# Performance work log

Measured on AMD Instinct MI355X. Metric: run time of the kernel, lower is better.

The kernel has to match this reference:

```python
import jax, jax.numpy as jnp
import numpy as np

N_DST = 50000


def setup_inputs() -> dict:
    key = jax.random.key(0)
    k1, k2, k3, k4, k5, k6 = jax.random.split(key, 6)
    n_src, n_dst, n_edges, d_in, d_out = 50000, 50000, 1600000, 128, 128
    return {
        "h_neigh": jax.random.normal(k1, (n_src, d_in), dtype=jnp.float32),
        "h_self": jax.random.normal(k2, (n_dst, d_in), dtype=jnp.float32),
        "src_idx": jax.random.randint(k3, (n_edges,), 0, n_src, dtype=jnp.int32),
        "dst_idx": jax.random.randint(k4, (n_edges,), 0, n_dst, dtype=jnp.int32),
        "W_self": jax.random.normal(k5, (d_out, d_in), dtype=jnp.float32) * 0.05,
        "W_neigh": jax.random.normal(k6, (d_out, d_in), dtype=jnp.float32) * 0.05,
    }


def reference(h_neigh, h_self, src_idx, dst_idx, W_self, W_neigh):
    # mean aggregation over edges: for each dst node, mean of src features
    msgs = h_neigh[src_idx]                                   # [E, d_in]
    summed = jax.ops.segment_sum(msgs, dst_idx, num_segments=N_DST)  # [N_dst, d_in]
    deg = jax.ops.segment_sum(jnp.ones_like(dst_idx, dtype=h_neigh.dtype),
                              dst_idx, num_segments=N_DST)    # [N_dst]
    agg = summed / jnp.maximum(deg, 1.0)[:, None]             # mean; 0 for isolated nodes

    z = h_self @ W_self.T + agg @ W_neigh.T                   # [N_dst, d_out]
    z = jax.nn.relu(z)
    # L2 normalize rows, guarding zero norms
    z_norm = jnp.linalg.norm(z, axis=1, keepdims=True)
    z_norm = jnp.where(z_norm == 0, 1.0, z_norm)
    return z / z_norm
```

## Files before the change

kernel.cpp:

```cpp
#include <hip/hip_runtime.h>
#include <hip/hip_bf16.h>

#define DFEAT 128
#define BSH 7
#define CAP 4608

typedef short short8 __attribute__((ext_vector_type(8)));
typedef float f32x4 __attribute__((ext_vector_type(4)));

__global__ void prep_kernel(const float2* __restrict__ in, __hip_bfloat162* __restrict__ out,
                            int n2, int nconv,
                            const float* __restrict__ Wself, const float* __restrict__ Wneigh,
                            unsigned short* __restrict__ wcat, int* __restrict__ gcursor) {
    int b = blockIdx.x;
    int tid = threadIdx.x;
    if (b < nconv) {
        int i = b * 256 + tid;
        if (i < n2) {
            float2 v = in[i];
            __hip_bfloat162 o;
            o.x = __float2bfloat16(v.x);
            o.y = __float2bfloat16(v.y);
            out[i] = o;
        }
    } else {
        int bb = b - nconv;
        int idx = bb * 256 + tid;
        int j = idx >> 8, k = idx & 255;
        float v = (k < DFEAT) ? Wself[j * DFEAT + k] : Wneigh[j * DFEAT + k - DFEAT];
        __hip_bfloat16 h = __float2bfloat16(v);
        wcat[idx] = *(unsigned short*)&h;
        if (bb < 2) {
            int s = bb * 256 + tid;
            gcursor[s] = s * CAP;
        }
    }
}

__global__ void partition_kernel(const int* __restrict__ src, const int* __restrict__ dst,
                                 int E, int* __restrict__ gcursor,
                                 unsigned* __restrict__ pairs) {
    __shared__ int hist[512];
    __shared__ int base[512];
    int tid = threadIdx.x;
    for (int b0 = blockIdx.x * 2048; b0 < E; b0 += gridDim.x * 2048) {
        hist[tid] = 0;
        hist[tid + 256] = 0;
        __syncthreads();
        unsigned mypk[8];
        int mybin[8], myrank[8];
#pragma unroll
        for (int e = 0; e < 8; ++e) {
            int i = b0 + e * 256 + tid;
            mybin[e] = -1;
            if (i < E) {
                unsigned d = (unsigned)dst[i];
                unsigned s = (unsigned)src[i];
                int bin = d >> BSH;
                mybin[e] = bin;
                myrank[e] = atomicAdd(&hist[bin], 1);
                mypk[e] = (d << 16) | s;
            }
        }
        __syncthreads();
        if (hist[tid]) base[tid] = atomicAdd(&gcursor[tid], hist[tid]);
        if (hist[tid + 256]) base[tid + 256] = atomicAdd(&gcursor[tid + 256], hist[tid + 256]);
        __syncthreads();
#pragma unroll
        for (int e = 0; e < 8; ++e)
            if (mybin[e] >= 0) pairs[base[mybin[e]] + myrank[e]] = mypk[e];
        __syncthreads();
    }
}

__global__ void fine_fill_kernel(const unsigned* __restrict__ pairs,
                                 const int* __restrict__ gcursor,
                                 int* __restrict__ row_start, int* __restrict__ deg,
                                 unsigned short* __restrict__ csr16, int n_dst) {
    __shared__ int hist[256];
    __shared__ int cur[256];
    __shared__ int wtot[4];
    int b = blockIdx.x;
    int tid = threadIdx.x;
    int lo = b * CAP, hi = gcursor[b];
    hist[tid] = 0;
    __syncthreads();
    for (int j = lo + tid; j < hi; j += 256)
        atomicAdd(&hist[(pairs[j] >> 16) & 127], 1);
    __syncthreads();
    int v = hist[tid];
    int lane = tid & 63, w = tid >> 6;
    int x = v;
    for (int off = 1; off < 64; off <<= 1) {
        int t = __shfl_up(x, off);
        if (lane >= off) x += t;
    }
    if (lane == 63) wtot[w] = x;
    __syncthreads();
    if (tid == 0) {
        int r = 0;
        for (int i = 0; i < 4; ++i) { int t = wtot[i]; wtot[i] = r; r += t; }
    }
    __syncthreads();
    int excl = x + wtot[w] - v;
    cur[tid] = excl;
    int d = (b << BSH) + tid;
    if (tid < (1 << BSH) && d < n_dst) {
        row_start[d] = lo + excl;
        deg[d] = v;
    }
    __syncthreads();
    for (int j = lo + tid; j < hi; j += 256) {
        unsigned p = pairs[j];
        int slot = atomicAdd(&cur[(p >> 16) & 127], 1);
        csr16[lo + slot] = (unsigned short)(p & 0xFFFFu);
    }
}

template <int PASS>
__global__ void aggregate_kernel(const unsigned short* __restrict__ hnb,
                                 const unsigned short* __restrict__ csr16,
                                 const int* __restrict__ row_start,
                                 const int* __restrict__ deg,
                                 unsigned short* __restrict__ agb, int n_dst) {
    int gtid = blockIdx.x * blockDim.x + threadIdx.x;
    int d = gtid >> 6;
    if (d >= n_dst) return;
    int lane = threadIdx.x & 63;
    int beg = row_start[d];
    int dg = deg[d];
    int slot = lane >> 4;
    int fg = lane & 15;
    const unsigned short* tab = hnb + PASS * 64 + fg * 4;
    float a0 = 0.f, a1 = 0.f, a2 = 0.f, a3 = 0.f;
    for (int base = 0; base < dg; base += 64) {
        int cnt = dg - base;
        if (cnt > 64) cnt = 64;
        int s = (base + lane < dg) ? (int)csr16[beg + base + lane] : 0;
        for (int j = 0; j < cnt; j += 8) {
            int e0 = j + slot;
            int e1 = e0 + 4;
            int i0 = __shfl(s, e0);
            int i1 = __shfl(s, e1 & 63);
            ushort4 v0 = *(const ushort4*)(tab + i0 * DFEAT);
            ushort4 v1 = *(const ushort4*)(tab + i1 * DFEAT);
            if (e0 < cnt) {
                a0 += __bfloat162float(*(__hip_bfloat16*)&v0.x);
                a1 += __bfloat162float(*(__hip_bfloat16*)&v0.y);
                a2 += __bfloat162float(*(__hip_bfloat16*)&v0.z);
                a3 += __bfloat162float(*(__hip_bfloat16*)&v0.w);
            }
            if (e1 < cnt) {
                a0 += __bfloat162float(*(__hip_bfloat16*)&v1.x);
                a1 += __bfloat162float(*(__hip_bfloat16*)&v1.y);
                a2 += __bfloat162float(*(__hip_bfloat16*)&v1.z);
                a3 += __bfloat162float(*(__hip_bfloat16*)&v1.w);
            }
        }
    }
    a0 += __shfl_xor(a0, 16); a0 += __shfl_xor(a0, 32);
    a1 += __shfl_xor(a1, 16); a1 += __shfl_xor(a1, 32);
    a2 += __shfl_xor(a2, 16); a2 += __shfl_xor(a2, 32);
    a3 += __shfl_xor(a3, 16); a3 += __shfl_xor(a3, 32);
    if (lane < 16) {
        float inv = 1.0f / (float)(dg > 1 ? dg : 1);
        __hip_bfloat16 b0 = __float2bfloat16(a0 * inv);
        __hip_bfloat16 b1 = __float2bfloat16(a1 * inv);
        __hip_bfloat16 b2 = __float2bfloat16(a2 * inv);
        __hip_bfloat16 b3 = __float2bfloat16(a3 * inv);
        ushort4 o;
        o.x = *(unsigned short*)&b0;
        o.y = *(unsigned short*)&b1;
        o.z = *(unsigned short*)&b2;
        o.w = *(unsigned short*)&b3;
        *(ushort4*)(agb + d * DFEAT + PASS * 64 + lane * 4) = o;
    }
}

__launch_bounds__(512, 4)
__global__ void gemm_mfma_kernel(const float* __restrict__ h_self,
                                 const unsigned short* __restrict__ agb,
                                 const unsigned short* __restrict__ Wcat,
                                 float* __restrict__ out, int M) {
    __shared__ char Ws[64 * 1024];
    int tid = threadIdx.x;
    int row0 = blockIdx.x * 128;
    {
        int j = tid >> 2, q = tid & 3;
#pragma unroll
        for (int u = 0; u < 8; ++u) {
            int ks = q * 64 + u * 8;
            uint4 vv = *(const uint4*)(Wcat + j * 256 + ks);
            *(uint4*)(Ws + ((j * 512 + ks * 2) ^ ((j & 7) << 4))) = vv;
        }
    }
    __syncthreads();

    int lane = tid & 63, w = tid >> 6;
    int arow = row0 + w * 16 + (lane & 15);
    int kgrp = (lane >> 4) * 8;
    bool rv = arow < M;
    int ar = rv ? arow : 0;

    f32x4 acc[8] = {};
#pragma unroll
    for (int kstep = 0; kstep < 8; ++kstep) {
        int kk = kstep * 32 + kgrp;
        short8 a;
        if (kk < DFEAT) {
            float4 f0 = *(const float4*)(h_self + (size_t)ar * DFEAT + kk);
            float4 f1 = *(const float4*)(h_self + (size_t)ar * DFEAT + kk + 4);
            __hip_bfloat16 b0 = __float2bfloat16(f0.x), b1 = __float2bfloat16(f0.y);
            __hip_bfloat16 b2 = __float2bfloat16(f0.z), b3 = __float2bfloat16(f0.w);
            __hip_bfloat16 b4 = __float2bfloat16(f1.x), b5 = __float2bfloat16(f1.y);
            __hip_bfloat16 b6 = __float2bfloat16(f1.z), b7 = __float2bfloat16(f1.w);
            a[0] = *(short*)&b0; a[1] = *(short*)&b1; a[2] = *(short*)&b2; a[3] = *(short*)&b3;
            a[4] = *(short*)&b4; a[5] = *(short*)&b5; a[6] = *(short*)&b6; a[7] = *(short*)&b7;
        } else {
            a = *(const short8*)(agb + (size_t)ar * DFEAT + (kk - DFEAT));
        }
#pragma unroll
        for (int n = 0; n < 8; ++n) {
            int nr = n * 16 + (lane & 15);
            short8 bfrag = *(const short8*)(Ws + ((nr * 512 + kk * 2) ^ ((nr & 7) << 4)));
            acc[n] = __builtin_amdgcn_mfma_f32_16x16x32_bf16(a, bfrag, acc[n], 0, 0, 0);
        }
    }

    float ss[4] = {0.f, 0.f, 0.f, 0.f};
#pragma unroll
    for (int n = 0; n < 8; ++n)
#pragma unroll
        for (int i = 0; i < 4; ++i) {
            float z = fmaxf(acc[n][i], 0.f);
            acc[n][i] = z;
            ss[i] += z * z;
        }
#pragma unroll
    for (int i = 0; i < 4; ++i)
        for (int m = 1; m < 16; m <<= 1) ss[i] += __shfl_xor(ss[i], m);
#pragma unroll
    for (int i = 0; i < 4; ++i) {
        int grow = row0 + w * 16 + (lane >> 4) * 4 + i;
        if (grow < M) {
            float nv = sqrtf(ss[i]);
            float inv = (nv == 0.f) ? 1.f : 1.f / nv;
#pragma unroll
            for (int n = 0; n < 8; ++n)
                out[(size_t)grow * DFEAT + n * 16 + (lane & 15)] = acc[n][i] * inv;
        }
    }
}

extern "C" void kernel_launch(void* const* d_in, const int* in_sizes, int n_in,
                              void* d_out, int out_size, void* d_ws, size_t ws_size,
                              hipStream_t stream) {
    const float* h_neigh = (const float*)d_in[0];
    const float* h_self  = (const float*)d_in[1];
    const int*   src_idx = (const int*)d_in[2];
    const int*   dst_idx = (const int*)d_in[3];
    const float* W_self  = (const float*)d_in[4];
    const float* W_neigh = (const float*)d_in[5];
    float* out = (float*)d_out;

    const int D = DFEAT;
    int n_src = in_sizes[0] / D;
    int n_dst = in_sizes[1] / D;
    int E = in_sizes[2];
    int NB = (n_dst + (1 << BSH) - 1) >> BSH;

    char* wsp = (char*)d_ws;
    size_t off = 0;
    auto alloc = [&](size_t bytes) -> void* {
        void* p = wsp + off;
        off += (bytes + 255) & ~(size_t)255;
        return p;
    };
    int* gcursor          = (int*)alloc(512 * 4);
    int* row_start        = (int*)alloc((size_t)n_dst * 4);
    int* deg              = (int*)alloc((size_t)n_dst * 4);
    unsigned* pairs       = (unsigned*)alloc((size_t)NB * CAP * 4);
    unsigned short* csr16 = (unsigned short*)alloc((size_t)NB * CAP * 2 + 256);
    unsigned short* hnb   = (unsigned short*)alloc((size_t)n_src * D * 2);
    unsigned short* agb   = (unsigned short*)alloc((size_t)n_dst * D * 2);
    unsigned short* wcat  = (unsigned short*)alloc((size_t)DFEAT * 256 * 2);
    (void)ws_size;

    int n2 = n_src * (D / 2);
    int nconv = (n2 + 255) / 256;
    prep_kernel<<<nconv + 128, 256, 0, stream>>>(
        (const float2*)h_neigh, (__hip_bfloat162*)hnb, n2, nconv,
        W_self, W_neigh, wcat, gcursor);

    partition_kernel<<<256, 256, 0, stream>>>(src_idx, dst_idx, E, gcursor, pairs);

    fine_fill_kernel<<<NB, 256, 0, stream>>>(pairs, gcursor, row_start, deg, csr16, n_dst);

    int agg_blocks = (n_dst * 64 + 255) / 256;
    aggregate_kernel<0><<<agg_blocks, 256, 0, stream>>>(hnb, csr16, row_start, deg, agb, n_dst);
    aggregate_kernel<1><<<agg_blocks, 256, 0, stream>>>(hnb, csr16, row_start, deg, agb, n_dst);

    gemm_mfma_kernel<<<(n_dst + 127) / 128, 512, 0, stream>>>(
        h_self, agb, wcat, out, n_dst);
}
```

Before: 130.4 us.

## Widen aggregate gathers to 16-byte loads with zero-row padding; vectorize partition index loads

The aggregate kernel now has each lane gather 8 bf16 features (16 bytes) instead of 4, with 8 edge slots per wavefront and four independent gathers per iteration. Padded edge slots point at an appended all-zero row of the bf16 neighbor table, so per-edge bounds branches disappear. The partition kernel reads src/dst as int4 vectors with contiguous per-thread edge ranges instead of strided scalar loads. This trades more wasted gather work on padded slots and higher register use for fewer, wider memory transactions and more memory-level parallelism.

```diff
diff --git a/kernel.cpp b/kernel.cpp
--- a/kernel.cpp
+++ b/kernel.cpp
@@ -6,10 +6,11 @@
 #define CAP 4608
 
 typedef short short8 __attribute__((ext_vector_type(8)));
+typedef unsigned short ushort8 __attribute__((ext_vector_type(8)));
 typedef float f32x4 __attribute__((ext_vector_type(4)));
 
 __global__ void prep_kernel(const float2* __restrict__ in, __hip_bfloat162* __restrict__ out,
-                            int n2, int nconv,
+                            int n2, int nconv, int n_src,
                             const float* __restrict__ Wself, const float* __restrict__ Wneigh,
                             unsigned short* __restrict__ wcat, int* __restrict__ gcursor) {
     int b = blockIdx.x;
@@ -34,6 +35,9 @@
             int s = bb * 256 + tid;
             gcursor[s] = s * CAP;
         }
+        if (bb == 2 && tid < DFEAT) {
+            ((unsigned short*)out)[(size_t)n_src * DFEAT + tid] = 0;
+        }
     }
 }
 
@@ -47,19 +51,36 @@
         hist[tid] = 0;
         hist[tid + 256] = 0;
         __syncthreads();
+        int eb = b0 + tid * 8;
+        int ss[8], dd[8];
+        if (eb + 8 <= E) {
+            int4 s0 = *(const int4*)(src + eb);
+            int4 s1 = *(const int4*)(src + eb + 4);
+            int4 d0 = *(const int4*)(dst + eb);
+            int4 d1 = *(const int4*)(dst + eb + 4);
+            ss[0] = s0.x; ss[1] = s0.y; ss[2] = s0.z; ss[3] = s0.w;
+            ss[4] = s1.x; ss[5] = s1.y; ss[6] = s1.z; ss[7] = s1.w;
+            dd[0] = d0.x; dd[1] = d0.y; dd[2] = d0.z; dd[3] = d0.w;
+            dd[4] = d1.x; dd[5] = d1.y; dd[6] = d1.z; dd[7] = d1.w;
+        } else {
+#pragma unroll
+            for (int e = 0; e < 8; ++e) {
+                int i = eb + e;
+                ss[e] = (i < E) ? src[i] : 0;
+                dd[e] = (i < E) ? dst[i] : -1;
+            }
+        }
         unsigned mypk[8];
         int mybin[8], myrank[8];
 #pragma unroll
         for (int e = 0; e < 8; ++e) {
-            int i = b0 + e * 256 + tid;
             mybin[e] = -1;
-            if (i < E) {
-                unsigned d = (unsigned)dst[i];
-                unsigned s = (unsigned)src[i];
+            if (eb + e < E) {
+                unsigned d = (unsigned)dd[e];
                 int bin = d >> BSH;
                 mybin[e] = bin;
                 myrank[e] = atomicAdd(&hist[bin], 1);
-                mypk[e] = (d << 16) | s;
+                mypk[e] = (d << 16) | (unsigned)ss[e];
             }
         }
         __syncthreads();
@@ -122,58 +143,55 @@
                                  const unsigned short* __restrict__ csr16,
                                  const int* __restrict__ row_start,
                                  const int* __restrict__ deg,
-                                 unsigned short* __restrict__ agb, int n_dst) {
+                                 unsigned short* __restrict__ agb, int n_dst, int zrow) {
     int gtid = blockIdx.x * blockDim.x + threadIdx.x;
     int d = gtid >> 6;
     if (d >= n_dst) return;
     int lane = threadIdx.x & 63;
     int beg = row_start[d];
     int dg = deg[d];
-    int slot = lane >> 4;
-    int fg = lane & 15;
-    const unsigned short* tab = hnb + PASS * 64 + fg * 4;
-    float a0 = 0.f, a1 = 0.f, a2 = 0.f, a3 = 0.f;
+    int slot = lane >> 3;
+    int fl = lane & 7;
+    const unsigned short* tab = hnb + PASS * 64 + fl * 8;
+    float a[8] = {0.f, 0.f, 0.f, 0.f, 0.f, 0.f, 0.f, 0.f};
     for (int base = 0; base < dg; base += 64) {
-        int cnt = dg - base;
-        if (cnt > 64) cnt = 64;
-        int s = (base + lane < dg) ? (int)csr16[beg + base + lane] : 0;
-        for (int j = 0; j < cnt; j += 8) {
-            int e0 = j + slot;
-            int e1 = e0 + 4;
-            int i0 = __shfl(s, e0);
-            int i1 = __shfl(s, e1 & 63);
-            ushort4 v0 = *(const ushort4*)(tab + i0 * DFEAT);
-            ushort4 v1 = *(const ushort4*)(tab + i1 * DFEAT);
-            if (e0 < cnt) {
-                a0 += __bfloat162float(*(__hip_bfloat16*)&v0.x);
-                a1 += __bfloat162float(*(__hip_bfloat16*)&v0.y);
-                a2 += __bfloat162float(*(__hip_bfloat16*)&v0.z);
-                a3 += __bfloat162float(*(__hip_bfloat16*)&v0.w);
-            }
-            if (e1 < cnt) {
-                a0 += __bfloat162float(*(__hip_bfloat16*)&v1.x);
-                a1 += __bfloat162float(*(__hip_bfloat16*)&v1.y);
-                a2 += __bfloat162float(*(__hip_bfloat16*)&v1.z);
-                a3 += __bfloat162float(*(__hip_bfloat16*)&v1.w);
-            }
-        }
-    }
-    a0 += __shfl_xor(a0, 16); a0 += __shfl_xor(a0, 32);
-    a1 += __shfl_xor(a1, 16); a1 += __shfl_xor(a1, 32);
-    a2 += __shfl_xor(a2, 16); a2 += __shfl_xor(a2, 32);
-    a3 += __shfl_xor(a3, 16); a3 += __shfl_xor(a3, 32);
-    if (lane < 16) {
+        int s = (base + lane < dg) ? (int)csr16[beg + base + lane] : zrow;
+        int lim = dg - base;
+        if (lim > 64) lim = 64;
+        for (int j = 0; j < lim; j += 32) {
+            int i0 = __shfl(s, j + slot);
+            int i1 = __shfl(s, j + 8 + slot);
+            int i2 = __shfl(s, j + 16 + slot);
+            int i3 = __shfl(s, j + 24 + slot);
+            ushort8 v0 = *(const ushort8*)(tab + (size_t)i0 * DFEAT);
+            ushort8 v1 = *(const ushort8*)(tab + (size_t)i1 * DFEAT);
+            ushort8 v2 = *(const ushort8*)(tab + (size_t)i2 * DFEAT);
+            ushort8 v3 = *(const ushort8*)(tab + (size_t)i3 * DFEAT);
+#pragma unroll
+            for (int k = 0; k < 8; ++k) a[k] += __uint_as_float((unsigned)v0[k] << 16);
+#pragma unroll
+            for (int k = 0; k < 8; ++k) a[k] += __uint_as_float((unsigned)v1[k] << 16);
+#pragma unroll
+            for (int k = 0; k < 8; ++k) a[k] += __uint_as_float((unsigned)v2[k] << 16);
+#pragma unroll
+            for (int k = 0; k < 8; ++k) a[k] += __uint_as_float((unsigned)v3[k] << 16);
+        }
+    }
+#pragma unroll
+    for (int k = 0; k < 8; ++k) {
+        a[k] += __shfl_xor(a[k], 8);
+        a[k] += __shfl_xor(a[k], 16);
+        a[k] += __shfl_xor(a[k], 32);
+    }
+    if (lane < 8) {
         float inv = 1.0f / (float)(dg > 1 ? dg : 1);
-        __hip_bfloat16 b0 = __float2bfloat16(a0 * inv);
-        __hip_bfloat16 b1 = __float2bfloat16(a1 * inv);
-        __hip_bfloat16 b2 = __float2bfloat16(a2 * inv);
-        __hip_bfloat16 b3 = __float2bfloat16(a3 * inv);
-        ushort4 o;
-        o.x = *(unsigned short*)&b0;
-        o.y = *(unsigned short*)&b1;
-        o.z = *(unsigned short*)&b2;
-        o.w = *(unsigned short*)&b3;
-        *(ushort4*)(agb + d * DFEAT + PASS * 64 + lane * 4) = o;
+        ushort8 o;
+#pragma unroll
+        for (int k = 0; k < 8; ++k) {
+            __hip_bfloat16 h = __float2bfloat16(a[k] * inv);
+            o[k] = *(unsigned short*)&h;
+        }
+        *(ushort8*)(agb + (size_t)d * DFEAT + PASS * 64 + lane * 8) = o;
     }
 }
 
@@ -281,7 +299,7 @@
     int* deg              = (int*)alloc((size_t)n_dst * 4);
     unsigned* pairs       = (unsigned*)alloc((size_t)NB * CAP * 4);
     unsigned short* csr16 = (unsigned short*)alloc((size_t)NB * CAP * 2 + 256);
-    unsigned short* hnb   = (unsigned short*)alloc((size_t)n_src * D * 2);
+    unsigned short* hnb   = (unsigned short*)alloc((size_t)(n_src + 1) * D * 2);
     unsigned short* agb   = (unsigned short*)alloc((size_t)n_dst * D * 2);
     unsigned short* wcat  = (unsigned short*)alloc((size_t)DFEAT * 256 * 2);
     (void)ws_size;
@@ -289,7 +307,7 @@
     int n2 = n_src * (D / 2);
     int nconv = (n2 + 255) / 256;
     prep_kernel<<<nconv + 128, 256, 0, stream>>>(
-        (const float2*)h_neigh, (__hip_bfloat162*)hnb, n2, nconv,
+        (const float2*)h_neigh, (__hip_bfloat162*)hnb, n2, nconv, n_src,
         W_self, W_neigh, wcat, gcursor);
 
     partition_kernel<<<256, 256, 0, stream>>>(src_idx, dst_idx, E, gcursor, pairs);
@@ -297,8 +315,8 @@
     fine_fill_kernel<<<NB, 256, 0, stream>>>(pairs, gcursor, row_start, deg, csr16, n_dst);
 
     int agg_blocks = (n_dst * 64 + 255) / 256;
-    aggregate_kernel<0><<<agg_blocks, 256, 0, stream>>>(hnb, csr16, row_start, deg, agb, n_dst);
-    aggregate_kernel<1><<<agg_blocks, 256, 0, stream>>>(hnb, csr16, row_start, deg, agb, n_dst);
+    aggregate_kernel<0><<<agg_blocks, 256, 0, stream>>>(hnb, csr16, row_start, deg, agb, n_dst, n_src);
+    aggregate_kernel<1><<<agg_blocks, 256, 0, stream>>>(hnb, csr16, row_start, deg, agb, n_dst, n_src);
 
     gemm_mfma_kernel<<<(n_dst + 127) / 128, 512, 0, stream>>>(
         h_self, agb, wcat, out, n_dst);
```

Measured after the change: 114.3 us. 12.3% less time.
